# Performance work log

Measured on AMD Instinct MI355X. Metric: run time of the kernel, lower is better.

Reference implementation:

```python
import jax, jax.numpy as jnp
import numpy as np
from jax.ops import segment_sum, segment_max

B, P, NP, EP = 128, 16, 256, 1280
EPG, ODIM, NH = 2048, 256, 128
EPS = 1e-5


def _bn(x, g, b):
    # BatchNorm1d (training-mode batch statistics), biased variance like torch
    mu = x.mean(0)
    var = ((x - mu) ** 2).mean(0)
    return g * (x - mu) * jax.lax.rsqrt(var + EPS) + b


def _gat(feat, src, dst, W, al, ar, resW, bias):
    # DGL GATConv: fc -> per-head attn logits -> leaky_relu -> edge softmax over dst -> aggregate; + residual fc + bias
    n = feat.shape[0]
    H, D = al.shape
    z = (feat @ W).reshape(n, H, D)
    el = (z * al).sum(-1)                                  # [n,H]
    er = (z * ar).sum(-1)
    e = jax.nn.leaky_relu(el[src] + er[dst], 0.2)          # [E,H]
    m = segment_max(e, dst, num_segments=n)
    ex = jnp.exp(e - m[dst])
    s = segment_sum(ex, dst, num_segments=n)
    a = ex / (s[dst] + 1e-9)
    rst = segment_sum(a[:, :, None] * z[src], dst, num_segments=n)  # [n,H,D]
    res = (feat @ resW).reshape(n, H, D)
    return (rst + res + bias.reshape(1, H, D)).reshape(n, H * D)


def _plane(feat, src, dst, p):
    # PlaneGraphEncoder forward (eval: dropout off)
    h = _gat(feat, src, dst, p['W1'], p['al1'], p['ar1'], p['res1'], p['b1'])
    h = jax.nn.relu(_bn(h, p['g1'], p['be1']))
    h = _gat(h, src, dst, p['W2'], p['al2'], p['ar2'], p['res2'], p['b2'])
    h = jax.nn.relu(_bn(h, p['g2'], p['be2']))
    rep = h.mean(0)                                        # dgl.mean_nodes -> [32]
    d = jax.nn.relu(_bn(h @ p['dW1'] + p['db1'], p['dg'], p['dbe']))
    recon = d @ p['dW2'] + p['db2']                        # [n,1]
    rloss = jnp.mean((recon - feat) ** 2)
    return rep, rloss


def _masked_gc(h, src, dst, mask_f, W, b):
    # DGL GraphConv(norm='both') with edge_weight = mask[src]*mask[dst]; structural degrees, clamp>=1
    n = h.shape[0]
    ones = jnp.ones(src.shape[0], h.dtype)
    d_out = jnp.maximum(segment_sum(ones, src, num_segments=n), 1.0)
    d_in = jnp.maximum(segment_sum(ones, dst, num_segments=n), 1.0)
    ew = mask_f[src] * mask_f[dst]                         # [E]
    hs = h * jax.lax.rsqrt(d_out)[:, None]
    agg = segment_sum(ew[:, None] * hs[src], dst, num_segments=n)
    return (agg * jax.lax.rsqrt(d_in)[:, None]) @ W + b


def _forward(plane_feat, original_features,
             W1, al1, ar1, res1, b1, g1, be1,
             W2, al2, ar2, res2, b2, g2, be2,
             dW1, db1, dg, dbe, dW2, db2,
             ft_W, ft_b, ft_g, ft_be, gc_W, gc_b, gbn_g, gbn_be,
             c1_W, c1_b, ln_g, ln_be, c2_W, c2_b,
             plane_src, plane_dst, patient_src, patient_dst, mask):
    pp = dict(W1=W1, al1=al1, ar1=ar1, res1=res1, b1=b1, g1=g1, be1=be1,
              W2=W2, al2=al2, ar2=ar2, res2=res2, b2=b2, g2=g2, be2=be2,
              dW1=dW1, db1=db1, dg=dg, dbe=dbe, dW2=dW2, db2=db2)
    enc_b = jax.vmap(_plane, in_axes=(0, 0, 0, None))      # over patients
    enc_pb = jax.vmap(enc_b, in_axes=(1, 1, 1, 0))         # over planes (params axis 0)
    reps, rlosses = enc_pb(plane_feat, plane_src, plane_dst, pp)   # [P,B,32], [P,B]
    plane_rep = jnp.transpose(reps, (1, 0, 2)).reshape(plane_feat.shape[0], -1)  # [B, P*32]
    avg_recon = rlosses.mean()                             # sum / (B*P)

    x = jnp.concatenate([original_features, plane_rep], axis=1)   # [B, fused]
    h = jax.nn.relu(_bn(x @ ft_W + ft_b, ft_g, ft_be))
    mask_f = mask.astype(h.dtype)
    h_sum = h
    for i in range(3):
        hn = _masked_gc(h, patient_src, patient_dst, mask_f, gc_W[i], gc_b[i])
        hn = jax.nn.relu(_bn(hn, gbn_g[i], gbn_be[i]))
        h = hn + h
        h_sum = h_sum + h
    h = h_sum / 4.0                                        # mean over [h0,h1,h2,h3]

    z = h @ c1_W + c1_b
    mu = z.mean(-1, keepdims=True)
    var = ((z - mu) ** 2).mean(-1, keepdims=True)
    z = jax.nn.relu(ln_g * (z - mu) * jax.lax.rsqrt(var + EPS) + ln_be)
    logits = z @ c2_W + c2_b
    return logits, avg_recon


def setup_inputs() -> dict:
    key = jax.random.key(0)
    ks = iter(jax.random.split(key, 64))
    f = lambda shape, s=0.1: jax.random.normal(next(ks), shape, jnp.float32) * s
    inp = dict(
        plane_feat=f((B, P, NP, 1), 1.0),
        plane_src=jax.random.randint(next(ks), (B, P, EP), 0, NP, jnp.int32),
        plane_dst=jax.random.randint(next(ks), (B, P, EP), 0, NP, jnp.int32),
        patient_src=jax.random.randint(next(ks), (EPG,), 0, B, jnp.int32),
        patient_dst=jax.random.randint(next(ks), (EPG,), 0, B, jnp.int32),
        original_features=f((B, ODIM), 1.0),
        mask=jax.random.randint(next(ks), (B,), 0, 2, jnp.int32),
        # per-plane encoder params, stacked over P
        W1=f((P, 1, 128)), al1=f((P, 2, 64)), ar1=f((P, 2, 64)),
        res1=f((P, 1, 128)), b1=f((P, 128)),
        g1=jnp.ones((P, 128)), be1=jnp.zeros((P, 128)),
        W2=f((P, 128, 32)), al2=f((P, 1, 32)), ar2=f((P, 1, 32)),
        res2=f((P, 128, 32)), b2=f((P, 32)),
        g2=jnp.ones((P, 32)), be2=jnp.zeros((P, 32)),
        dW1=f((P, 32, 128)), db1=f((P, 128)),
        dg=jnp.ones((P, 128)), dbe=jnp.zeros((P, 128)),
        dW2=f((P, 128, 1)), db2=f((P, 1)),
        # patient-level params
        ft_W=f((ODIM + P * 32, NH)), ft_b=f((NH,)),
        ft_g=jnp.ones((NH,)), ft_be=jnp.zeros((NH,)),
        gc_W=f((3, NH, NH)), gc_b=f((3, NH)),
        gbn_g=jnp.ones((3, NH)), gbn_be=jnp.zeros((3, NH)),
        c1_W=f((NH, NH // 2)), c1_b=f((NH // 2,)),
        ln_g=jnp.ones((NH // 2,)), ln_be=jnp.zeros((NH // 2,)),
        c2_W=f((NH // 2, 2)), c2_b=f((2,)),
    )
    return inp


def reference(plane_feat, plane_src, plane_dst, patient_src, patient_dst,
              original_features, mask,
              W1, al1, ar1, res1, b1, g1, be1,
              W2, al2, ar2, res2, b2, g2, be2,
              dW1, db1, dg, dbe, dW2, db2,
              ft_W, ft_b, ft_g, ft_be, gc_W, gc_b, gbn_g, gbn_be,
              c1_W, c1_b, ln_g, ln_be, c2_W, c2_b):
    return _forward(plane_feat, original_features,
                    W1, al1, ar1, res1, b1, g1, be1,
                    W2, al2, ar2, res2, b2, g2, be2,
                    dW1, db1, dg, dbe, dW2, db2,
                    ft_W, ft_b, ft_g, ft_be, gc_W, gc_b, gbn_g, gbn_be,
                    c1_W, c1_b, ln_g, ln_be, c2_W, c2_b,
                    plane_src, plane_dst, patient_src, patient_dst, mask)
```

## Files before the change

kernel.cpp:

```cpp
#include <hip/hip_runtime.h>

#define B_    128
#define P_    16
#define NP_   256
#define EP_   1280
#define EPG_  2048
#define ODIM_ 256
#define NH_   128

typedef __attribute__((ext_vector_type(8))) short s8_t;
typedef __attribute__((ext_vector_type(4))) float f4_t;

__device__ __forceinline__ unsigned short f2b(float x) {
  unsigned u = __builtin_bit_cast(unsigned, x);
  u = (u + 0x7fffu + ((u >> 16) & 1u)) >> 16;
  return (unsigned short)u;
}
__device__ __forceinline__ float b2f(short x) {
  unsigned u = ((unsigned)(unsigned short)x) << 16;
  return __builtin_bit_cast(float, u);
}

struct SmemA {
  float f[256];
  float S0a[256], S1a[256];
  float el2[256], er2[256];
  float abg0[128], abg1[128], abg2[128];
  float al2v[32], ar2v[32];
  __align__(16) unsigned short wT[64 * 136];
  __align__(16) unsigned short z2[256 * 40];
  int cnt[256]; int wtot[4];
  unsigned short esrc[1280];
  float redf[512];
  float scA[32], shA[32];
  float dscA[64], dshA[64];
  float dW2v[128];
  float r8[4][8]; float stat[8]; float wA[2], wB[2];
  float rlacc;
};

__global__ __launch_bounds__(256, 3) void plane_enc(
    const float* __restrict__ feat, const int* __restrict__ esrcg, const int* __restrict__ edstg,
    const float* __restrict__ W1, const float* __restrict__ al1, const float* __restrict__ ar1,
    const float* __restrict__ res1, const float* __restrict__ b1, const float* __restrict__ g1,
    const float* __restrict__ be1,
    const float* __restrict__ W2, const float* __restrict__ al2, const float* __restrict__ ar2,
    const float* __restrict__ res2, const float* __restrict__ g2, const float* __restrict__ be2,
    const float* __restrict__ dW1, const float* __restrict__ dg, const float* __restrict__ dbe,
    const float* __restrict__ dW2, const float* __restrict__ db2,
    float* __restrict__ rep_out, float* __restrict__ rloss_out)
{
  __shared__ SmemA s;
  const int g = blockIdx.x;
  const int p = g & 15;
  const int t = threadIdx.x;
  const int lane = t & 63, wv = t >> 6;
  const int l15 = lane & 15, quad = lane >> 4;

  s.f[t] = feat[g * NP_ + t];
  if (t < 32) { s.al2v[t] = al2[p * 32 + t]; s.ar2v[t] = ar2[p * 32 + t]; }
  if (t == 0) s.rlacc = 0.f;
  s.cnt[t] = 0;
  __syncthreads();

  const int* gs = esrcg + g * EP_;
  const int* gd = edstg + g * EP_;
  for (int k = t; k < EP_; k += 256) atomicAdd(&s.cnt[gd[k]], 1);
  __syncthreads();
  int v = s.cnt[t];
  int incl = v;
  #pragma unroll
  for (int off = 1; off < 64; off <<= 1) {
    int n = __shfl_up(incl, off, 64);
    if (lane >= off) incl += n;
  }
  if (lane == 63) s.wtot[wv] = incl;
  __syncthreads();
  int woff = 0;
  for (int w = 0; w < wv; w++) woff += s.wtot[w];
  const int myStart = woff + incl - v;
  const int myDeg = v;
  __syncthreads();
  s.cnt[t] = myStart;
  __syncthreads();
  for (int k = t; k < EP_; k += 256) {
    int d = gd[k];
    int pos = atomicAdd(&s.cnt[d], 1);
    s.esrc[pos] = (unsigned short)gs[k];
  }
  {
    const float* W2g = W2 + p * 4096;
    const float* Rg  = res2 + p * 4096;
    for (int q = 0; q < 16; q++) {
      int idx = t + 256 * q;
      int k = idx >> 5, n = idx & 31;
      s.wT[n * 136 + k]        = f2b(W2g[idx]);
      s.wT[(n + 32) * 136 + k] = f2b(Rg[idx]);
    }
  }
  if (t < 128) {
    float w1v = W1[p * 128 + t];
    s.el2[t] = w1v * al1[p * 128 + t];
    s.er2[t] = w1v * ar1[p * 128 + t];
  }
  __syncthreads();
  if (t < 2) {
    float a = 0.f, bq = 0.f;
    for (int d2 = 0; d2 < 64; d2++) { a += s.el2[t * 64 + d2]; bq += s.er2[t * 64 + d2]; }
    s.wA[t] = a; s.wB[t] = bq;
  }
  __syncthreads();

  const float fi = s.f[t];
  float S0, S1;
  {
    const float wa0 = s.wA[0], wb0 = s.wB[0], wa1 = s.wA[1], wb1 = s.wB[1];
    float m0 = -1e30f, m1 = -1e30f;
    for (int j = 0; j < myDeg; j++) {
      float fs = s.f[s.esrc[myStart + j]];
      float e0 = wa0 * fs + wb0 * fi; e0 = e0 > 0.f ? e0 : 0.2f * e0;
      float e1 = wa1 * fs + wb1 * fi; e1 = e1 > 0.f ? e1 : 0.2f * e1;
      m0 = fmaxf(m0, e0); m1 = fmaxf(m1, e1);
    }
    float ss0 = 0.f, ss1 = 0.f, U0 = 0.f, U1 = 0.f;
    for (int j = 0; j < myDeg; j++) {
      float fs = s.f[s.esrc[myStart + j]];
      float e0 = wa0 * fs + wb0 * fi; e0 = e0 > 0.f ? e0 : 0.2f * e0;
      float e1 = wa1 * fs + wb1 * fi; e1 = e1 > 0.f ? e1 : 0.2f * e1;
      float x0 = __expf(e0 - m0), x1 = __expf(e1 - m1);
      ss0 += x0; U0 += x0 * fs;
      ss1 += x1; U1 += x1 * fs;
    }
    S0 = U0 / (ss0 + 1e-9f);
    S1 = U1 / (ss1 + 1e-9f);
    s.S0a[t] = S0; s.S1a[t] = S1;
  }

  {
    float vals[8] = {fi, fi * fi, S0, S0 * S0, S0 * fi, S1, S1 * S1, S1 * fi};
    #pragma unroll
    for (int d2 = 32; d2 > 0; d2 >>= 1) {
      #pragma unroll
      for (int q = 0; q < 8; q++) vals[q] += __shfl_down(vals[q], d2, 64);
    }
    if (lane == 0) {
      #pragma unroll
      for (int q = 0; q < 8; q++) s.r8[wv][q] = vals[q];
    }
  }
  __syncthreads();
  if (t < 8) s.stat[t] = (s.r8[0][t] + s.r8[1][t] + s.r8[2][t] + s.r8[3][t]) * (1.f / 256.f);
  __syncthreads();
  if (t < 128) {
    float mf = s.stat[0], ef2 = s.stat[1];
    int hh = t >> 6;
    float mS = s.stat[2 + 3 * hh], eS2 = s.stat[3 + 3 * hh], eSf = s.stat[4 + 3 * hh];
    float varS = eS2 - mS * mS, varf = ef2 - mf * mf, cov = eSf - mS * mf;
    float Wv = W1[p * 128 + t], Rv = res1[p * 128 + t], Bv = b1[p * 128 + t];
    float mu  = Wv * mS + Rv * mf + Bv;
    float var = Wv * Wv * varS + Rv * Rv * varf + 2.f * Wv * Rv * cov;
    float gn  = g1[p * 128 + t] * rsqrtf(var + 1e-5f);
    s.abg0[t] = gn * Wv;
    s.abg1[t] = gn * Rv;
    s.abg2[t] = gn * (Bv - mu) + be1[p * 128 + t];
  }
  __syncthreads();

  float resv[32];
  {
    f4_t accum[4][4];
    #pragma unroll
    for (int i = 0; i < 4; i++)
      #pragma unroll
      for (int nt = 0; nt < 4; nt++) accum[i][nt] = (f4_t){0.f, 0.f, 0.f, 0.f};

    float fm[4], s0m[4], s1m[4];
    #pragma unroll
    for (int i = 0; i < 4; i++) {
      int m = (wv * 4 + i) * 16 + l15;
      fm[i] = s.f[m]; s0m[i] = s.S0a[m]; s1m[i] = s.S1a[m];
    }
    #pragma unroll
    for (int kt = 0; kt < 4; kt++) {
      int cbase = kt * 32 + quad * 8;
      float a0[8], a1[8], a2[8];
      #pragma unroll
      for (int j = 0; j < 8; j++) {
        a0[j] = s.abg0[cbase + j]; a1[j] = s.abg1[cbase + j]; a2[j] = s.abg2[cbase + j];
      }
      s8_t afr[4];
      #pragma unroll
      for (int i = 0; i < 4; i++) {
        float Sm = (kt < 2) ? s0m[i] : s1m[i];
        union { s8_t v; unsigned short u[8]; } fu;
        #pragma unroll
        for (int j = 0; j < 8; j++) {
          float h = fmaxf(fmaf(a0[j], Sm, fmaf(a1[j], fm[i], a2[j])), 0.f);
          fu.u[j] = f2b(h);
        }
        afr[i] = fu.v;
      }
      s8_t bfr[4];
      #pragma unroll
      for (int nt = 0; nt < 4; nt++)
        bfr[nt] = *(const s8_t*)&s.wT[(nt * 16 + l15) * 136 + cbase];
      #pragma unroll
      for (int i = 0; i < 4; i++)
        #pragma unroll
        for (int nt = 0; nt < 4; nt++)
          accum[i][nt] = __builtin_amdgcn_mfma_f32_16x16x32_bf16(afr[i], bfr[nt], accum[i][nt], 0, 0, 0);
    }
    #pragma unroll
    for (int i = 0; i < 4; i++) {
      int mBase = (wv * 4 + i) * 16 + quad * 4;
      #pragma unroll
      for (int nt = 0; nt < 2; nt++) {
        int col = nt * 16 + l15;
        #pragma unroll
        for (int r = 0; r < 4; r++)
          s.z2[(mBase + r) * 40 + col] = f2b(accum[i][nt][r]);
      }
      #pragma unroll
      for (int h2 = 0; h2 < 2; h2++)
        #pragma unroll
        for (int r = 0; r < 4; r++)
          resv[(i * 2 + h2) * 4 + r] = accum[i][2 + h2][r];
    }
  }
  __syncthreads();

  {
    const s8_t* zr = (const s8_t*)&s.z2[t * 40];
    float el = 0.f, er = 0.f;
    #pragma unroll
    for (int q = 0; q < 4; q++) {
      s8_t vz = zr[q];
      #pragma unroll
      for (int j = 0; j < 8; j++) {
        float zv = b2f(vz[j]);
        el += zv * s.al2v[q * 8 + j];
        er += zv * s.ar2v[q * 8 + j];
      }
    }
    s.el2[t] = el; s.er2[t] = er;
  }
  {
    const float* Dg = dW1 + p * 4096;
    for (int q = 0; q < 16; q++) {
      int idx = t + 256 * q;
      int k = idx >> 7, n = idx & 127;
      s.wT[n * 40 + k] = f2b(Dg[idx]);
    }
    if (t < 128) s.dW2v[t] = dW2[p * 128 + t];
  }
  const float db2v = db2[p];
  __syncthreads();

  float hrow[32];
  {
    const float eri = s.er2[t];
    float m = -1e30f;
    for (int j = 0; j < myDeg; j++) {
      float e = s.el2[s.esrc[myStart + j]] + eri;
      e = e > 0.f ? e : 0.2f * e;
      m = fmaxf(m, e);
    }
    float ss = 0.f;
    #pragma unroll
    for (int d2 = 0; d2 < 32; d2++) hrow[d2] = 0.f;
    for (int j = 0; j < myDeg; j++) {
      int sj = s.esrc[myStart + j];
      float e = s.el2[sj] + eri;
      e = e > 0.f ? e : 0.2f * e;
      float x = __expf(e - m);
      ss += x;
      const s8_t* zr = (const s8_t*)&s.z2[sj * 40];
      #pragma unroll
      for (int q = 0; q < 4; q++) {
        s8_t vz = zr[q];
        #pragma unroll
        for (int jj = 0; jj < 8; jj++) hrow[q * 8 + jj] += x * b2f(vz[jj]);
      }
    }
    float inv = 1.f / (ss + 1e-9f);
    #pragma unroll
    for (int d2 = 0; d2 < 32; d2++) hrow[d2] *= inv;
  }
  __syncthreads();
  #pragma unroll
  for (int i = 0; i < 4; i++) {
    int mBase = (wv * 4 + i) * 16 + quad * 4;
    #pragma unroll
    for (int h2 = 0; h2 < 2; h2++) {
      int col = h2 * 16 + l15;
      #pragma unroll
      for (int r = 0; r < 4; r++)
        s.z2[(mBase + r) * 40 + col] = f2b(resv[(i * 2 + h2) * 4 + r]);
    }
  }
  __syncthreads();
  {
    const s8_t* zr = (const s8_t*)&s.z2[t * 40];
    #pragma unroll
    for (int q = 0; q < 4; q++) {
      s8_t vz = zr[q];
      #pragma unroll
      for (int jj = 0; jj < 8; jj++) hrow[q * 8 + jj] += b2f(vz[jj]);
    }
  }
  #pragma unroll
  for (int d2 = 0; d2 < 32; d2++) s.z2[t * 40 + d2] = f2b(hrow[d2]);
  __syncthreads();

  {
    int c = t & 31, gq = t >> 5;
    float s1 = 0.f, s2 = 0.f;
    for (int j = 0; j < 32; j++) {
      float vz = b2f((short)s.z2[(gq * 32 + j) * 40 + c]);
      s1 += vz; s2 += vz * vz;
    }
    s.redf[t] = s1; s.redf[256 + t] = s2;
  }
  __syncthreads();
  if (t < 32) {
    float s1 = 0.f, s2 = 0.f;
    #pragma unroll
    for (int q = 0; q < 8; q++) { s1 += s.redf[q * 32 + t]; s2 += s.redf[256 + q * 32 + t]; }
    float mu = s1 * (1.f / 256.f);
    float var = s2 * (1.f / 256.f) - mu * mu;
    float a = g2[p * 32 + t] * rsqrtf(var + 1e-5f);
    s.scA[t] = a; s.shA[t] = be2[p * 32 + t] - a * mu;
  }
  __syncthreads();
  {
    int c = t & 31, gq = t >> 5;
    float a = s.scA[c], bb = s.shA[c];
    float s1 = 0.f;
    for (int j = 0; j < 32; j++) {
      int ad = (gq * 32 + j) * 40 + c;
      float vz = b2f((short)s.z2[ad]);
      float hv = fmaxf(a * vz + bb, 0.f);
      s.z2[ad] = f2b(hv);
      s1 += hv;
    }
    s.redf[t] = s1;
  }
  __syncthreads();
  if (t < 32) {
    float s1 = 0.f;
    #pragma unroll
    for (int q = 0; q < 8; q++) s1 += s.redf[q * 32 + t];
    rep_out[g * 32 + t] = s1 * (1.f / 256.f);
  }
  __syncthreads();

  {
    s8_t afr2[4];
    #pragma unroll
    for (int i = 0; i < 4; i++)
      afr2[i] = *(const s8_t*)&s.z2[((wv * 4 + i) * 16 + l15) * 40 + quad * 8];
    float rAcc[4][4];
    #pragma unroll
    for (int i = 0; i < 4; i++)
      #pragma unroll
      for (int r = 0; r < 4; r++) rAcc[i][r] = 0.f;

    for (int half = 0; half < 2; half++) {
      __syncthreads();
      s.redf[t] = 0.f; s.redf[256 + t] = 0.f;
      __syncthreads();
      f4_t acc2[4][4];
      #pragma unroll
      for (int i = 0; i < 4; i++)
        #pragma unroll
        for (int nt = 0; nt < 4; nt++) acc2[i][nt] = (f4_t){0.f, 0.f, 0.f, 0.f};
      s8_t bfr[4];
      #pragma unroll
      for (int nt = 0; nt < 4; nt++)
        bfr[nt] = *(const s8_t*)&s.wT[(half * 64 + nt * 16 + l15) * 40 + quad * 8];
      #pragma unroll
      for (int i = 0; i < 4; i++)
        #pragma unroll
        for (int nt = 0; nt < 4; nt++)
          acc2[i][nt] = __builtin_amdgcn_mfma_f32_16x16x32_bf16(afr2[i], bfr[nt], acc2[i][nt], 0, 0, 0);
      #pragma unroll
      for (int nt = 0; nt < 4; nt++) {
        float s1 = 0.f, s2 = 0.f;
        #pragma unroll
        for (int i = 0; i < 4; i++)
          #pragma unroll
          for (int r = 0; r < 4; r++) { float vv = acc2[i][nt][r]; s1 += vv; s2 += vv * vv; }
        atomicAdd(&s.redf[nt * 16 + l15], s1);
        atomicAdd(&s.redf[256 + nt * 16 + l15], s2);
      }
      __syncthreads();
      if (t < 64) {
        int col = half * 64 + t;
        float mu = s.redf[t] * (1.f / 256.f);
        float var = s.redf[256 + t] * (1.f / 256.f) - mu * mu;
        float a = dg[p * 128 + col] * rsqrtf(var + 1e-5f);
        s.dscA[t] = a; s.dshA[t] = dbe[p * 128 + col] - a * mu;
      }
      __syncthreads();
      #pragma unroll
      for (int nt = 0; nt < 4; nt++) {
        int cl = nt * 16 + l15;
        float a = s.dscA[cl], bb = s.dshA[cl], w2 = s.dW2v[half * 64 + cl];
        #pragma unroll
        for (int i = 0; i < 4; i++)
          #pragma unroll
          for (int r = 0; r < 4; r++) {
            float dv = fmaxf(a * acc2[i][nt][r] + bb, 0.f);
            rAcc[i][r] += dv * w2;
          }
      }
    }
    #pragma unroll
    for (int off = 1; off < 16; off <<= 1)
      #pragma unroll
      for (int i = 0; i < 4; i++)
        #pragma unroll
        for (int r = 0; r < 4; r++) rAcc[i][r] += __shfl_xor(rAcc[i][r], off, 64);
    if (l15 == 0) {
      float sq = 0.f;
      #pragma unroll
      for (int i = 0; i < 4; i++)
        #pragma unroll
        for (int r = 0; r < 4; r++) {
          int m = (wv * 4 + i) * 16 + quad * 4 + r;
          float diff = rAcc[i][r] + db2v - s.f[m];
          sq += diff * diff;
        }
      atomicAdd(&s.rlacc, sq);
    }
  }
  __syncthreads();
  if (t == 0) atomicAdd(rloss_out, s.rlacc * (1.f / (256.f * 2048.f)));
}

struct SmemB {
  __align__(16) unsigned short arow[128 * 136];
  __align__(16) unsigned short hT[128 * 136];
  union {
    float aB[128 * 132];
    struct {
      union {
        __align__(16) unsigned short wT[128 * 136];
        float zF[128 * 68];
      } w;
      __align__(16) unsigned short aggB[128 * 136];
    } mm;
  } u;
  float redA[1024], redB[1024];
  float facs[128], facd[128], scB[128], shB[128];
  int co[128], ci[128];
};

__global__ __launch_bounds__(1024) void k_patient(
    const float* __restrict__ orig, const float* __restrict__ rep,
    const float* __restrict__ ftW, const float* __restrict__ ftg, const float* __restrict__ ftbe,
    const int* __restrict__ ps, const int* __restrict__ pd, const int* __restrict__ mask,
    const float* __restrict__ gcW, const float* __restrict__ gbng, const float* __restrict__ gbnbe,
    const float* __restrict__ c1W, const float* __restrict__ c1b,
    const float* __restrict__ lng, const float* __restrict__ lnbe,
    const float* __restrict__ c2W, const float* __restrict__ c2b,
    const float* __restrict__ rl, float* __restrict__ out)
{
  __shared__ SmemB s;
  const int t = threadIdx.x;
  const int w = t >> 6, lane = t & 63;
  const int l15 = lane & 15, quad = lane >> 4;
  const int mb = w & 7, nb = (w >> 3) * 64;

  if (t < 128) { s.co[t] = 0; s.ci[t] = 0; }
  for (int idx = t; idx < 128 * 132; idx += 1024) s.u.aB[idx] = 0.f;
  __syncthreads();
  for (int e = t; e < EPG_; e += 1024) { atomicAdd(&s.co[ps[e]], 1); atomicAdd(&s.ci[pd[e]], 1); }
  __syncthreads();
  if (t < 128) {
    float mk = (float)mask[t];
    int da = s.co[t] > 1 ? s.co[t] : 1;
    int db = s.ci[t] > 1 ? s.ci[t] : 1;
    s.facs[t] = mk * rsqrtf((float)da);
    s.facd[t] = mk * rsqrtf((float)db);
  }
  for (int e = t; e < EPG_; e += 1024) atomicAdd(&s.u.aB[pd[e] * 132 + ps[e]], 1.f);
  __syncthreads();
  for (int idx = t; idx < 16384; idx += 1024) {
    int d = idx >> 7, sN = idx & 127;
    s.arow[d * 136 + sN] = f2b(s.u.aB[d * 132 + sN] * s.facd[d] * s.facs[sN]);
  }
  __syncthreads();

  f4_t acc[4];
  #pragma unroll
  for (int nt = 0; nt < 4; nt++) acc[nt] = (f4_t){0.f, 0.f, 0.f, 0.f};
  const int m = mb * 16 + l15;
  for (int chunk = 0; chunk < 6; chunk++) {
    #pragma unroll
    for (int q = 0; q < 16; q++) {
      int idx = t + 1024 * q;
      int kk = idx >> 7, n = idx & 127;
      s.u.mm.w.wT[n * 136 + kk] = f2b(ftW[(chunk * 128 + kk) * 128 + n]);
    }
    __syncthreads();
    #pragma unroll
    for (int ks = 0; ks < 4; ks++) {
      int k0 = chunk * 128 + ks * 32 + quad * 8;
      const float* px = (k0 < 256) ? (orig + m * 256 + k0) : (rep + m * 512 + (k0 - 256));
      float4 xa = ((const float4*)px)[0];
      float4 xb = ((const float4*)px)[1];
      union { s8_t v; unsigned short u[8]; } fu;
      fu.u[0] = f2b(xa.x); fu.u[1] = f2b(xa.y); fu.u[2] = f2b(xa.z); fu.u[3] = f2b(xa.w);
      fu.u[4] = f2b(xb.x); fu.u[5] = f2b(xb.y); fu.u[6] = f2b(xb.z); fu.u[7] = f2b(xb.w);
      #pragma unroll
      for (int nt = 0; nt < 4; nt++) {
        s8_t bfr = *(const s8_t*)&s.u.mm.w.wT[(nb + nt * 16 + l15) * 136 + ks * 32 + quad * 8];
        acc[nt] = __builtin_amdgcn_mfma_f32_16x16x32_bf16(fu.v, bfr, acc[nt], 0, 0, 0);
      }
    }
    __syncthreads();
  }

  float hR[16], hsumR[16];
  {
    #pragma unroll
    for (int nt = 0; nt < 4; nt++) {
      float s1 = acc[nt][0] + acc[nt][1] + acc[nt][2] + acc[nt][3];
      float s2 = acc[nt][0]*acc[nt][0] + acc[nt][1]*acc[nt][1] + acc[nt][2]*acc[nt][2] + acc[nt][3]*acc[nt][3];
      s1 += __shfl_xor(s1, 16, 64); s1 += __shfl_xor(s1, 32, 64);
      s2 += __shfl_xor(s2, 16, 64); s2 += __shfl_xor(s2, 32, 64);
      if (quad == 0) {
        s.redA[mb * 128 + nb + nt * 16 + l15] = s1;
        s.redB[mb * 128 + nb + nt * 16 + l15] = s2;
      }
    }
    __syncthreads();
    if (t < 128) {
      float a1 = 0.f, a2 = 0.f;
      #pragma unroll
      for (int q = 0; q < 8; q++) { a1 += s.redA[q * 128 + t]; a2 += s.redB[q * 128 + t]; }
      float mu = a1 * (1.f / 128.f), var = a2 * (1.f / 128.f) - mu * mu;
      float a = ftg[t] * rsqrtf(var + 1e-5f);
      s.scB[t] = a; s.shB[t] = ftbe[t] - a * mu;
    }
    __syncthreads();
    #pragma unroll
    for (int nt = 0; nt < 4; nt++) {
      int col = nb + nt * 16 + l15;
      float a = s.scB[col], bb = s.shB[col];
      #pragma unroll
      for (int r = 0; r < 4; r++) {
        int row = mb * 16 + quad * 4 + r;
        float hv = fmaxf(a * acc[nt][r] + bb, 0.f);
        hR[nt * 4 + r] = hv; hsumR[nt * 4 + r] = hv;
        s.hT[col * 136 + row] = f2b(hv);
      }
    }
  }
  __syncthreads();

  for (int layer = 0; layer < 3; layer++) {
    #pragma unroll
    for (int q = 0; q < 16; q++) {
      int idx = t + 1024 * q;
      int kk = idx >> 7, n = idx & 127;
      s.u.mm.w.wT[n * 136 + kk] = f2b(gcW[layer * 16384 + kk * 128 + n]);
    }
    f4_t ag[4];
    #pragma unroll
    for (int nt = 0; nt < 4; nt++) ag[nt] = (f4_t){0.f, 0.f, 0.f, 0.f};
    #pragma unroll
    for (int ks = 0; ks < 4; ks++) {
      s8_t afr = *(const s8_t*)&s.arow[(mb * 16 + l15) * 136 + ks * 32 + quad * 8];
      #pragma unroll
      for (int nt = 0; nt < 4; nt++) {
        s8_t bfr = *(const s8_t*)&s.hT[(nb + nt * 16 + l15) * 136 + ks * 32 + quad * 8];
        ag[nt] = __builtin_amdgcn_mfma_f32_16x16x32_bf16(afr, bfr, ag[nt], 0, 0, 0);
      }
    }
    #pragma unroll
    for (int nt = 0; nt < 4; nt++) {
      int col = nb + nt * 16 + l15;
      #pragma unroll
      for (int r = 0; r < 4; r++)
        s.u.mm.aggB[(mb * 16 + quad * 4 + r) * 136 + col] = f2b(ag[nt][r]);
    }
    __syncthreads();
    f4_t oc[4];
    #pragma unroll
    for (int nt = 0; nt < 4; nt++) oc[nt] = (f4_t){0.f, 0.f, 0.f, 0.f};
    #pragma unroll
    for (int ks = 0; ks < 4; ks++) {
      s8_t afr = *(const s8_t*)&s.u.mm.aggB[(mb * 16 + l15) * 136 + ks * 32 + quad * 8];
      #pragma unroll
      for (int nt = 0; nt < 4; nt++) {
        s8_t bfr = *(const s8_t*)&s.u.mm.w.wT[(nb + nt * 16 + l15) * 136 + ks * 32 + quad * 8];
        oc[nt] = __builtin_amdgcn_mfma_f32_16x16x32_bf16(afr, bfr, oc[nt], 0, 0, 0);
      }
    }
    #pragma unroll
    for (int nt = 0; nt < 4; nt++) {
      float s1 = oc[nt][0] + oc[nt][1] + oc[nt][2] + oc[nt][3];
      float s2 = oc[nt][0]*oc[nt][0] + oc[nt][1]*oc[nt][1] + oc[nt][2]*oc[nt][2] + oc[nt][3]*oc[nt][3];
      s1 += __shfl_xor(s1, 16, 64); s1 += __shfl_xor(s1, 32, 64);
      s2 += __shfl_xor(s2, 16, 64); s2 += __shfl_xor(s2, 32, 64);
      if (quad == 0) {
        s.redA[mb * 128 + nb + nt * 16 + l15] = s1;
        s.redB[mb * 128 + nb + nt * 16 + l15] = s2;
      }
    }
    __syncthreads();
    if (t < 128) {
      float a1 = 0.f, a2 = 0.f;
      #pragma unroll
      for (int q = 0; q < 8; q++) { a1 += s.redA[q * 128 + t]; a2 += s.redB[q * 128 + t]; }
      float mu = a1 * (1.f / 128.f), var = a2 * (1.f / 128.f) - mu * mu;
      float a = gbng[layer * 128 + t] * rsqrtf(var + 1e-5f);
      s.scB[t] = a; s.shB[t] = gbnbe[layer * 128 + t] - a * mu;
    }
    __syncthreads();
    #pragma unroll
    for (int nt = 0; nt < 4; nt++) {
      int col = nb + nt * 16 + l15;
      float a = s.scB[col], bb = s.shB[col];
      #pragma unroll
      for (int r = 0; r < 4; r++) {
        int row = mb * 16 + quad * 4 + r;
        float hn = fmaxf(a * oc[nt][r] + bb, 0.f) + hR[nt * 4 + r];
        hR[nt * 4 + r] = hn;
        hsumR[nt * 4 + r] += hn;
        s.hT[col * 136 + row] = f2b(hn);
      }
    }
    __syncthreads();
  }

  #pragma unroll
  for (int nt = 0; nt < 4; nt++) {
    int col = nb + nt * 16 + l15;
    #pragma unroll
    for (int r = 0; r < 4; r++)
      s.u.mm.aggB[(mb * 16 + quad * 4 + r) * 136 + col] = f2b(hsumR[nt * 4 + r] * 0.25f);
  }
  #pragma unroll
  for (int q = 0; q < 8; q++) {
    int idx = t + 1024 * q;
    int n = idx & 63, kk = idx >> 6;
    s.u.mm.w.wT[n * 136 + kk] = f2b(c1W[kk * 64 + n]);
  }
  __syncthreads();
  {
    const int nb2 = (w >> 3) * 32;
    f4_t zc[2];
    #pragma unroll
    for (int nt = 0; nt < 2; nt++) zc[nt] = (f4_t){0.f, 0.f, 0.f, 0.f};
    #pragma unroll
    for (int ks = 0; ks < 4; ks++) {
      s8_t afr = *(const s8_t*)&s.u.mm.aggB[(mb * 16 + l15) * 136 + ks * 32 + quad * 8];
      #pragma unroll
      for (int nt = 0; nt < 2; nt++) {
        s8_t bfr = *(const s8_t*)&s.u.mm.w.wT[(nb2 + nt * 16 + l15) * 136 + ks * 32 + quad * 8];
        zc[nt] = __builtin_amdgcn_mfma_f32_16x16x32_bf16(afr, bfr, zc[nt], 0, 0, 0);
      }
    }
    __syncthreads();
    #pragma unroll
    for (int nt = 0; nt < 2; nt++) {
      int col = nb2 + nt * 16 + l15;
      #pragma unroll
      for (int r = 0; r < 4; r++)
        s.u.mm.w.zF[(mb * 16 + quad * 4 + r) * 68 + col] = zc[nt][r] + c1b[col];
    }
  }
  __syncthreads();
  if (t < 128) {
    float s1 = 0.f, s2 = 0.f;
    #pragma unroll
    for (int j = 0; j < 64; j++) { float zv = s.u.mm.w.zF[t * 68 + j]; s1 += zv; s2 += zv * zv; }
    float mu = s1 * (1.f / 64.f);
    float var = s2 * (1.f / 64.f) - mu * mu;
    float rs = rsqrtf(var + 1e-5f);
    float l0 = 0.f, l1 = 0.f;
    #pragma unroll
    for (int j = 0; j < 64; j++) {
      float zv = s.u.mm.w.zF[t * 68 + j];
      float zn = fmaxf(lng[j] * (zv - mu) * rs + lnbe[j], 0.f);
      l0 += zn * c2W[j * 2];
      l1 += zn * c2W[j * 2 + 1];
    }
    out[t * 2]     = l0 + c2b[0];
    out[t * 2 + 1] = l1 + c2b[1];
  }
  if (t == 0) out[256] = rl[0];
}

extern "C" void kernel_launch(void* const* d_in, const int* in_sizes, int n_in,
                              void* d_out, int out_size, void* d_ws, size_t ws_size,
                              hipStream_t stream) {
  (void)in_sizes; (void)n_in; (void)out_size; (void)ws_size;
  const float* plane_feat  = (const float*)d_in[0];
  const int*   plane_src   = (const int*)d_in[1];
  const int*   plane_dst   = (const int*)d_in[2];
  const int*   patient_src = (const int*)d_in[3];
  const int*   patient_dst = (const int*)d_in[4];
  const float* orig        = (const float*)d_in[5];
  const int*   mask        = (const int*)d_in[6];
  const float* W1   = (const float*)d_in[7];
  const float* al1  = (const float*)d_in[8];
  const float* ar1  = (const float*)d_in[9];
  const float* res1 = (const float*)d_in[10];
  const float* b1   = (const float*)d_in[11];
  const float* g1   = (const float*)d_in[12];
  const float* be1  = (const float*)d_in[13];
  const float* W2   = (const float*)d_in[14];
  const float* al2  = (const float*)d_in[15];
  const float* ar2  = (const float*)d_in[16];
  const float* res2 = (const float*)d_in[17];
  const float* g2   = (const float*)d_in[19];
  const float* be2  = (const float*)d_in[20];
  const float* dW1  = (const float*)d_in[21];
  const float* dg   = (const float*)d_in[23];
  const float* dbe  = (const float*)d_in[24];
  const float* dW2  = (const float*)d_in[25];
  const float* db2  = (const float*)d_in[26];
  const float* ftW  = (const float*)d_in[27];
  const float* ftg  = (const float*)d_in[29];
  const float* ftbe = (const float*)d_in[30];
  const float* gcW  = (const float*)d_in[31];
  const float* gbng = (const float*)d_in[33];
  const float* gbnbe= (const float*)d_in[34];
  const float* c1W  = (const float*)d_in[35];
  const float* c1b  = (const float*)d_in[36];
  const float* lng  = (const float*)d_in[37];
  const float* lnbe = (const float*)d_in[38];
  const float* c2W  = (const float*)d_in[39];
  const float* c2b  = (const float*)d_in[40];

  float* ws   = (float*)d_ws;
  float* rep  = ws;
  float* rl   = ws + 131328;
  float* outp = (float*)d_out;

  hipMemsetAsync(rl, 0, sizeof(float), stream);
  plane_enc<<<2048, 256, 0, stream>>>(plane_feat, plane_src, plane_dst,
      W1, al1, ar1, res1, b1, g1, be1, W2, al2, ar2, res2, g2, be2,
      dW1, dg, dbe, dW2, db2, rep, rl);
  k_patient<<<1, 1024, 0, stream>>>(orig, rep, ftW, ftg, ftbe,
      patient_src, patient_dst, mask,
      gcW, gbng, gbnbe, c1W, c1b, lng, lnbe, c2W, c2b, rl, outp);
}
```

Baseline: 364.8 us.

## Offload patient weight transposes and adjacency build to extra plane_enc blocks

Adds nine extra blocks to the plane encoder grid that pre-transpose the ft, gc and c1 weights to bf16 and build the normalized patient adjacency in workspace. The single-block patient kernel then reads these operands straight from global memory instead of preparing them serially in LDS. The per-graph squared-error sums are written to a buffer and reduced in the patient kernel, replacing the global atomic and the memset launch. The cost is uncoalesced global fragment loads inside the single-block kernel in place of LDS reads.

```diff
diff --git a/kernel.cpp b/kernel.cpp
--- a/kernel.cpp
+++ b/kernel.cpp
@@ -20,6 +20,7 @@
   unsigned u = ((unsigned)(unsigned short)x) << 16;
   return __builtin_bit_cast(float, u);
 }
+
 
 struct SmemA {
   float f[256];
@@ -48,14 +49,73 @@
     const float* __restrict__ res2, const float* __restrict__ g2, const float* __restrict__ be2,
     const float* __restrict__ dW1, const float* __restrict__ dg, const float* __restrict__ dbe,
     const float* __restrict__ dW2, const float* __restrict__ db2,
-    float* __restrict__ rep_out, float* __restrict__ rloss_out)
+    const float* __restrict__ ftW, const float* __restrict__ gcW, const float* __restrict__ c1W,
+    const int* __restrict__ ps, const int* __restrict__ pd, const int* __restrict__ mask,
+    float* __restrict__ ws)
 {
   __shared__ SmemA s;
   const int g = blockIdx.x;
+  const int t = threadIdx.x;
+
+  if (g >= 2048) {
+    const int role = g - 2048;
+    unsigned short* ftT  = (unsigned short*)(ws + 67584);
+    unsigned short* gcT  = (unsigned short*)(ws + 116736);
+    unsigned short* c1T  = (unsigned short*)(ws + 141312);
+    unsigned short* abar = (unsigned short*)(ws + 145408);
+    if (role < 6) {
+      for (int idx = t; idx < 16384; idx += 256) {
+        int k = role * 128 + (idx >> 7), n = idx & 127;
+        ftT[n * 768 + k] = f2b(ftW[k * 128 + n]);
+      }
+    } else if (role == 6) {
+      for (int idx = t; idx < 49152; idx += 256) {
+        int l = idx >> 14, r = idx & 16383, k = r >> 7, n = r & 127;
+        gcT[l * 16384 + n * 128 + k] = f2b(gcW[l * 16384 + k * 128 + n]);
+      }
+    } else if (role == 7) {
+      for (int idx = t; idx < 8192; idx += 256) {
+        int k = idx >> 6, n = idx & 63;
+        c1T[n * 128 + k] = f2b(c1W[k * 64 + n]);
+      }
+    } else {
+      unsigned* cnt2 = (unsigned*)&s;
+      int* co = (int*)(cnt2 + 8192);
+      int* ci = co + 128;
+      float* facs = (float*)(ci + 128);
+      float* facd = facs + 128;
+      for (int idx = t; idx < 8192; idx += 256) cnt2[idx] = 0u;
+      if (t < 128) { co[t] = 0; ci[t] = 0; }
+      __syncthreads();
+      for (int e = t; e < EPG_; e += 256) {
+        int sN = ps[e], d = pd[e];
+        atomicAdd(&co[sN], 1); atomicAdd(&ci[d], 1);
+        int pair = d * 128 + sN;
+        atomicAdd(&cnt2[pair >> 1], 1u << ((pair & 1) * 16));
+      }
+      __syncthreads();
+      if (t < 128) {
+        float mk = (float)mask[t];
+        int da = co[t] > 1 ? co[t] : 1;
+        int db = ci[t] > 1 ? ci[t] : 1;
+        facs[t] = mk * rsqrtf((float)da);
+        facd[t] = mk * rsqrtf((float)db);
+      }
+      __syncthreads();
+      for (int idx = t; idx < 16384; idx += 256) {
+        int d = idx >> 7, sN = idx & 127;
+        unsigned cc = (cnt2[idx >> 1] >> ((idx & 1) * 16)) & 0xffffu;
+        abar[idx] = f2b((float)cc * facd[d] * facs[sN]);
+      }
+    }
+    return;
+  }
+
   const int p = g & 15;
-  const int t = threadIdx.x;
   const int lane = t & 63, wv = t >> 6;
   const int l15 = lane & 15, quad = lane >> 4;
+  float* rep_out = ws;
+  float* sq_out  = ws + 65536;
 
   s.f[t] = feat[g * NP_ + t];
   if (t < 32) { s.al2v[t] = al2[p * 32 + t]; s.ar2v[t] = ar2[p * 32 + t]; }
@@ -435,36 +495,28 @@
     }
   }
   __syncthreads();
-  if (t == 0) atomicAdd(rloss_out, s.rlacc * (1.f / (256.f * 2048.f)));
+  if (t == 0) sq_out[g] = s.rlacc;
 }
 
 struct SmemB {
-  __align__(16) unsigned short arow[128 * 136];
   __align__(16) unsigned short hT[128 * 136];
   union {
-    float aB[128 * 132];
-    struct {
-      union {
-        __align__(16) unsigned short wT[128 * 136];
-        float zF[128 * 68];
-      } w;
-      __align__(16) unsigned short aggB[128 * 136];
-    } mm;
+    __align__(16) unsigned short aggB[128 * 136];
+    float zF[128 * 68];
   } u;
   float redA[1024], redB[1024];
-  float facs[128], facd[128], scB[128], shB[128];
-  int co[128], ci[128];
+  float scB[128], shB[128];
+  float rsum[16];
 };
 
 __global__ __launch_bounds__(1024) void k_patient(
-    const float* __restrict__ orig, const float* __restrict__ rep,
-    const float* __restrict__ ftW, const float* __restrict__ ftg, const float* __restrict__ ftbe,
-    const int* __restrict__ ps, const int* __restrict__ pd, const int* __restrict__ mask,
-    const float* __restrict__ gcW, const float* __restrict__ gbng, const float* __restrict__ gbnbe,
-    const float* __restrict__ c1W, const float* __restrict__ c1b,
+    const float* __restrict__ orig, const float* __restrict__ ws_ro,
+    const float* __restrict__ ftg, const float* __restrict__ ftbe,
+    const float* __restrict__ gbng, const float* __restrict__ gbnbe,
+    const float* __restrict__ c1b,
     const float* __restrict__ lng, const float* __restrict__ lnbe,
     const float* __restrict__ c2W, const float* __restrict__ c2b,
-    const float* __restrict__ rl, float* __restrict__ out)
+    float* __restrict__ out)
 {
   __shared__ SmemB s;
   const int t = threadIdx.x;
@@ -472,38 +524,26 @@
   const int l15 = lane & 15, quad = lane >> 4;
   const int mb = w & 7, nb = (w >> 3) * 64;
 
-  if (t < 128) { s.co[t] = 0; s.ci[t] = 0; }
-  for (int idx = t; idx < 128 * 132; idx += 1024) s.u.aB[idx] = 0.f;
-  __syncthreads();
-  for (int e = t; e < EPG_; e += 1024) { atomicAdd(&s.co[ps[e]], 1); atomicAdd(&s.ci[pd[e]], 1); }
-  __syncthreads();
-  if (t < 128) {
-    float mk = (float)mask[t];
-    int da = s.co[t] > 1 ? s.co[t] : 1;
-    int db = s.ci[t] > 1 ? s.ci[t] : 1;
-    s.facs[t] = mk * rsqrtf((float)da);
-    s.facd[t] = mk * rsqrtf((float)db);
-  }
-  for (int e = t; e < EPG_; e += 1024) atomicAdd(&s.u.aB[pd[e] * 132 + ps[e]], 1.f);
-  __syncthreads();
-  for (int idx = t; idx < 16384; idx += 1024) {
-    int d = idx >> 7, sN = idx & 127;
-    s.arow[d * 136 + sN] = f2b(s.u.aB[d * 132 + sN] * s.facd[d] * s.facs[sN]);
-  }
-  __syncthreads();
+  const float* rep = ws_ro;
+  const float* sq  = ws_ro + 65536;
+  const unsigned short* ftT  = (const unsigned short*)(ws_ro + 67584);
+  const unsigned short* gcT  = (const unsigned short*)(ws_ro + 116736);
+  const unsigned short* c1T  = (const unsigned short*)(ws_ro + 141312);
+  const unsigned short* abar = (const unsigned short*)(ws_ro + 145408);
+
+  {
+    float v = sq[t] + sq[t + 1024];
+    #pragma unroll
+    for (int d2 = 32; d2 > 0; d2 >>= 1) v += __shfl_down(v, d2, 64);
+    if (lane == 0) s.rsum[w] = v;
+  }
 
   f4_t acc[4];
   #pragma unroll
   for (int nt = 0; nt < 4; nt++) acc[nt] = (f4_t){0.f, 0.f, 0.f, 0.f};
   const int m = mb * 16 + l15;
+  #pragma unroll 1
   for (int chunk = 0; chunk < 6; chunk++) {
-    #pragma unroll
-    for (int q = 0; q < 16; q++) {
-      int idx = t + 1024 * q;
-      int kk = idx >> 7, n = idx & 127;
-      s.u.mm.w.wT[n * 136 + kk] = f2b(ftW[(chunk * 128 + kk) * 128 + n]);
-    }
-    __syncthreads();
     #pragma unroll
     for (int ks = 0; ks < 4; ks++) {
       int k0 = chunk * 128 + ks * 32 + quad * 8;
@@ -515,64 +555,56 @@
       fu.u[4] = f2b(xb.x); fu.u[5] = f2b(xb.y); fu.u[6] = f2b(xb.z); fu.u[7] = f2b(xb.w);
       #pragma unroll
       for (int nt = 0; nt < 4; nt++) {
-        s8_t bfr = *(const s8_t*)&s.u.mm.w.wT[(nb + nt * 16 + l15) * 136 + ks * 32 + quad * 8];
+        s8_t bfr = *(const s8_t*)&ftT[(nb + nt * 16 + l15) * 768 + k0];
         acc[nt] = __builtin_amdgcn_mfma_f32_16x16x32_bf16(fu.v, bfr, acc[nt], 0, 0, 0);
       }
     }
-    __syncthreads();
   }
 
   float hR[16], hsumR[16];
-  {
-    #pragma unroll
-    for (int nt = 0; nt < 4; nt++) {
-      float s1 = acc[nt][0] + acc[nt][1] + acc[nt][2] + acc[nt][3];
-      float s2 = acc[nt][0]*acc[nt][0] + acc[nt][1]*acc[nt][1] + acc[nt][2]*acc[nt][2] + acc[nt][3]*acc[nt][3];
-      s1 += __shfl_xor(s1, 16, 64); s1 += __shfl_xor(s1, 32, 64);
-      s2 += __shfl_xor(s2, 16, 64); s2 += __shfl_xor(s2, 32, 64);
-      if (quad == 0) {
-        s.redA[mb * 128 + nb + nt * 16 + l15] = s1;
-        s.redB[mb * 128 + nb + nt * 16 + l15] = s2;
-      }
-    }
-    __syncthreads();
-    if (t < 128) {
-      float a1 = 0.f, a2 = 0.f;
-      #pragma unroll
-      for (int q = 0; q < 8; q++) { a1 += s.redA[q * 128 + t]; a2 += s.redB[q * 128 + t]; }
-      float mu = a1 * (1.f / 128.f), var = a2 * (1.f / 128.f) - mu * mu;
-      float a = ftg[t] * rsqrtf(var + 1e-5f);
-      s.scB[t] = a; s.shB[t] = ftbe[t] - a * mu;
-    }
-    __syncthreads();
-    #pragma unroll
-    for (int nt = 0; nt < 4; nt++) {
-      int col = nb + nt * 16 + l15;
-      float a = s.scB[col], bb = s.shB[col];
-      #pragma unroll
-      for (int r = 0; r < 4; r++) {
-        int row = mb * 16 + quad * 4 + r;
-        float hv = fmaxf(a * acc[nt][r] + bb, 0.f);
-        hR[nt * 4 + r] = hv; hsumR[nt * 4 + r] = hv;
-        s.hT[col * 136 + row] = f2b(hv);
-      }
-    }
-  }
-  __syncthreads();
-
+  #pragma unroll
+  for (int nt = 0; nt < 4; nt++) {
+    float s1 = acc[nt][0] + acc[nt][1] + acc[nt][2] + acc[nt][3];
+    float s2 = acc[nt][0]*acc[nt][0] + acc[nt][1]*acc[nt][1] + acc[nt][2]*acc[nt][2] + acc[nt][3]*acc[nt][3];
+    s1 += __shfl_xor(s1, 16, 64); s1 += __shfl_xor(s1, 32, 64);
+    s2 += __shfl_xor(s2, 16, 64); s2 += __shfl_xor(s2, 32, 64);
+    if (quad == 0) {
+      s.redA[mb * 128 + nb + nt * 16 + l15] = s1;
+      s.redB[mb * 128 + nb + nt * 16 + l15] = s2;
+    }
+  }
+  __syncthreads();
+  if (t < 128) {
+    float a1 = 0.f, a2 = 0.f;
+    #pragma unroll
+    for (int q = 0; q < 8; q++) { a1 += s.redA[q * 128 + t]; a2 += s.redB[q * 128 + t]; }
+    float mu = a1 * (1.f / 128.f), var = a2 * (1.f / 128.f) - mu * mu;
+    float a = ftg[t] * rsqrtf(var + 1e-5f);
+    s.scB[t] = a; s.shB[t] = ftbe[t] - a * mu;
+  }
+  __syncthreads();
+  #pragma unroll
+  for (int nt = 0; nt < 4; nt++) {
+    int col = nb + nt * 16 + l15;
+    float a = s.scB[col], bb = s.shB[col];
+    #pragma unroll
+    for (int r = 0; r < 4; r++) {
+      int row = mb * 16 + quad * 4 + r;
+      float hv = fmaxf(a * acc[nt][r] + bb, 0.f);
+      hR[nt * 4 + r] = hv; hsumR[nt * 4 + r] = hv;
+      s.hT[col * 136 + row] = f2b(hv);
+    }
+  }
+  __syncthreads();
+
+  #pragma unroll 1
   for (int layer = 0; layer < 3; layer++) {
-    #pragma unroll
-    for (int q = 0; q < 16; q++) {
-      int idx = t + 1024 * q;
-      int kk = idx >> 7, n = idx & 127;
-      s.u.mm.w.wT[n * 136 + kk] = f2b(gcW[layer * 16384 + kk * 128 + n]);
-    }
     f4_t ag[4];
     #pragma unroll
     for (int nt = 0; nt < 4; nt++) ag[nt] = (f4_t){0.f, 0.f, 0.f, 0.f};
     #pragma unroll
     for (int ks = 0; ks < 4; ks++) {
-      s8_t afr = *(const s8_t*)&s.arow[(mb * 16 + l15) * 136 + ks * 32 + quad * 8];
+      s8_t afr = *(const s8_t*)&abar[(mb * 16 + l15) * 128 + ks * 32 + quad * 8];
       #pragma unroll
       for (int nt = 0; nt < 4; nt++) {
         s8_t bfr = *(const s8_t*)&s.hT[(nb + nt * 16 + l15) * 136 + ks * 32 + quad * 8];
@@ -584,7 +616,7 @@
       int col = nb + nt * 16 + l15;
       #pragma unroll
       for (int r = 0; r < 4; r++)
-        s.u.mm.aggB[(mb * 16 + quad * 4 + r) * 136 + col] = f2b(ag[nt][r]);
+        s.u.aggB[(mb * 16 + quad * 4 + r) * 136 + col] = f2b(ag[nt][r]);
     }
     __syncthreads();
     f4_t oc[4];
@@ -592,10 +624,10 @@
     for (int nt = 0; nt < 4; nt++) oc[nt] = (f4_t){0.f, 0.f, 0.f, 0.f};
     #pragma unroll
     for (int ks = 0; ks < 4; ks++) {
-      s8_t afr = *(const s8_t*)&s.u.mm.aggB[(mb * 16 + l15) * 136 + ks * 32 + quad * 8];
+      s8_t afr = *(const s8_t*)&s.u.aggB[(mb * 16 + l15) * 136 + ks * 32 + quad * 8];
       #pragma unroll
       for (int nt = 0; nt < 4; nt++) {
-        s8_t bfr = *(const s8_t*)&s.u.mm.w.wT[(nb + nt * 16 + l15) * 136 + ks * 32 + quad * 8];
+        s8_t bfr = *(const s8_t*)&gcT[layer * 16384 + (nb + nt * 16 + l15) * 128 + ks * 32 + quad * 8];
         oc[nt] = __builtin_amdgcn_mfma_f32_16x16x32_bf16(afr, bfr, oc[nt], 0, 0, 0);
       }
     }
@@ -641,13 +673,7 @@
     int col = nb + nt * 16 + l15;
     #pragma unroll
     for (int r = 0; r < 4; r++)
-      s.u.mm.aggB[(mb * 16 + quad * 4 + r) * 136 + col] = f2b(hsumR[nt * 4 + r] * 0.25f);
-  }
-  #pragma unroll
-  for (int q = 0; q < 8; q++) {
-    int idx = t + 1024 * q;
-    int n = idx & 63, kk = idx >> 6;
-    s.u.mm.w.wT[n * 136 + kk] = f2b(c1W[kk * 64 + n]);
+      s.u.aggB[(mb * 16 + quad * 4 + r) * 136 + col] = f2b(hsumR[nt * 4 + r] * 0.25f);
   }
   __syncthreads();
   {
@@ -657,10 +683,10 @@
     for (int nt = 0; nt < 2; nt++) zc[nt] = (f4_t){0.f, 0.f, 0.f, 0.f};
     #pragma unroll
     for (int ks = 0; ks < 4; ks++) {
-      s8_t afr = *(const s8_t*)&s.u.mm.aggB[(mb * 16 + l15) * 136 + ks * 32 + quad * 8];
+      s8_t afr = *(const s8_t*)&s.u.aggB[(mb * 16 + l15) * 136 + ks * 32 + quad * 8];
       #pragma unroll
       for (int nt = 0; nt < 2; nt++) {
-        s8_t bfr = *(const s8_t*)&s.u.mm.w.wT[(nb2 + nt * 16 + l15) * 136 + ks * 32 + quad * 8];
+        s8_t bfr = *(const s8_t*)&c1T[(nb2 + nt * 16 + l15) * 128 + ks * 32 + quad * 8];
         zc[nt] = __builtin_amdgcn_mfma_f32_16x16x32_bf16(afr, bfr, zc[nt], 0, 0, 0);
       }
     }
@@ -670,21 +696,21 @@
       int col = nb2 + nt * 16 + l15;
       #pragma unroll
       for (int r = 0; r < 4; r++)
-        s.u.mm.w.zF[(mb * 16 + quad * 4 + r) * 68 + col] = zc[nt][r] + c1b[col];
+        s.u.zF[(mb * 16 + quad * 4 + r) * 68 + col] = zc[nt][r] + c1b[col];
     }
   }
   __syncthreads();
   if (t < 128) {
     float s1 = 0.f, s2 = 0.f;
     #pragma unroll
-    for (int j = 0; j < 64; j++) { float zv = s.u.mm.w.zF[t * 68 + j]; s1 += zv; s2 += zv * zv; }
+    for (int j = 0; j < 64; j++) { float zv = s.u.zF[t * 68 + j]; s1 += zv; s2 += zv * zv; }
     float mu = s1 * (1.f / 64.f);
     float var = s2 * (1.f / 64.f) - mu * mu;
     float rs = rsqrtf(var + 1e-5f);
     float l0 = 0.f, l1 = 0.f;
     #pragma unroll
     for (int j = 0; j < 64; j++) {
-      float zv = s.u.mm.w.zF[t * 68 + j];
+      float zv = s.u.zF[t * 68 + j];
       float zn = fmaxf(lng[j] * (zv - mu) * rs + lnbe[j], 0.f);
       l0 += zn * c2W[j * 2];
       l1 += zn * c2W[j * 2 + 1];
@@ -692,7 +718,12 @@
     out[t * 2]     = l0 + c2b[0];
     out[t * 2 + 1] = l1 + c2b[1];
   }
-  if (t == 0) out[256] = rl[0];
+  if (t == 0) {
+    float tot = 0.f;
+    #pragma unroll
+    for (int q = 0; q < 16; q++) tot += s.rsum[q];
+    out[256] = tot * (1.f / (256.f * 2048.f));
+  }
 }
 
 extern "C" void kernel_launch(void* const* d_in, const int* in_sizes, int n_in,
@@ -738,15 +769,12 @@
   const float* c2b  = (const float*)d_in[40];
 
   float* ws   = (float*)d_ws;
-  float* rep  = ws;
-  float* rl   = ws + 131328;
   float* outp = (float*)d_out;
 
-  hipMemsetAsync(rl, 0, sizeof(float), stream);
-  plane_enc<<<2048, 256, 0, stream>>>(plane_feat, plane_src, plane_dst,
+  plane_enc<<<2057, 256, 0, stream>>>(plane_feat, plane_src, plane_dst,
       W1, al1, ar1, res1, b1, g1, be1, W2, al2, ar2, res2, g2, be2,
-      dW1, dg, dbe, dW2, db2, rep, rl);
-  k_patient<<<1, 1024, 0, stream>>>(orig, rep, ftW, ftg, ftbe,
-      patient_src, patient_dst, mask,
-      gcW, gbng, gbnbe, c1W, c1b, lng, lnbe, c2W, c2b, rl, outp);
+      dW1, dg, dbe, dW2, db2,
+      ftW, gcW, c1W, patient_src, patient_dst, mask, ws);
+  k_patient<<<1, 1024, 0, stream>>>(orig, ws, ftg, ftbe, gbng, gbnbe,
+      c1b, lng, lnbe, c2W, c2b, outp);
 }
```

After: 403.8 us. 10.7% more time.
